# Kernel tuning notes

Hardware: AMD Instinct MI355X
Metric: run time of the kernel (lower is better)

Reference implementation:

```python
import jax, jax.numpy as jnp
import numpy as np

EPS = 1e-5
RATIO = (0.25, 0.25)
PATCH = (8, 8)
GROUPS = 8


def dct_matrix(N):
    # Orthonormal DCT-II matrix: dct_2d(x, norm='ortho') == C @ x @ C.T
    n = jnp.arange(N, dtype=jnp.float32)
    C = jnp.cos(jnp.pi * (n[None, :] + 0.5) * n[:, None] / N)
    s = jnp.where(n == 0, jnp.sqrt(1.0 / N), jnp.sqrt(2.0 / N))
    return C * s[:, None]


def dct2(x, Ch, Cw):
    y = jnp.einsum('uh,nchw->ncuw', Ch, x)
    return jnp.einsum('ncuw,vw->ncuv', y, Cw)


def idct2(x, Ch, Cw):
    y = jnp.einsum('hu,ncuv->nchv', Ch, x)
    return jnp.einsum('nchv,wv->nchw', y, Cw)


def conv2d(x, w, b=None, groups=1):
    y = jax.lax.conv_general_dilated(x, w, (1, 1), 'SAME',
        dimension_numbers=('NCHW', 'OIHW', 'NCHW'), feature_group_count=groups)
    return y if b is None else y + b[None, :, None, None]


def channel_norm(x, g, b):
    # GroupNorm with num_groups == num_channels (per-channel instance norm)
    mu = x.mean(axis=(2, 3), keepdims=True)
    var = ((x - mu) ** 2).mean(axis=(2, 3), keepdims=True)
    return (x - mu) * jax.lax.rsqrt(var + EPS) * g[None, :, None, None] + b[None, :, None, None]


def dwt(x):
    x01 = x[:, :, 0::2, :]
    x02 = x[:, :, 1::2, :]
    x1 = x01[:, :, :, 0::2]
    x2 = x02[:, :, :, 0::2]
    x3 = x01[:, :, :, 1::2]
    x4 = x02[:, :, :, 1::2]
    LL = (x1 + x2 + x3 + x4) / 4
    HL = (-x1 - x2 + x3 + x4) / 4
    LH = (-x1 + x2 - x3 + x4) / 4
    HH = (x1 - x2 - x3 + x4) / 4
    return LL, HL, LH, HH


def idwt(LL, HL, LH, HH):
    x1 = LL - HL - LH + HH
    x2 = LL - HL + LH - HH
    x3 = LL + HL - LH - HH
    x4 = LL + HL + LH + HH
    b, c, h, w = x1.shape
    upper = jnp.zeros((b, c, 2 * h, w), x1.dtype).at[:, :, 0::2, :].set(x1).at[:, :, 1::2, :].set(x2)
    lower = jnp.zeros((b, c, 2 * h, w), x1.dtype).at[:, :, 0::2, :].set(x3).at[:, :, 1::2, :].set(x4)
    return jnp.zeros((b, c, 2 * h, 2 * w), x1.dtype).at[:, :, :, 0::2].set(upper).at[:, :, :, 1::2].set(lower)


def freq_mask(h, w):
    h0, w0 = int(h * RATIO[0]), int(w * RATIO[1])
    return jnp.ones((h, w), jnp.float32).at[:h0, :w0].set(0.0)


def spatial_branch(x, noise_thr):
    LL, HL, LH, HH = dwt(x)
    h0, w0 = LL.shape[2], LL.shape[3]
    Ch, Cw = dct_matrix(h0), dct_matrix(w0)
    d = dct2(LL, Ch, Cw)
    d = jnp.where(jnp.abs(d) > noise_thr, jnp.tanh(d), d)
    d = d * freq_mask(h0, w0)[None, None]
    dct_ = idct2(d, Ch, Cw)
    return idwt(LL * dct_, HL * dct_, LH * dct_, HH * dct_)


def channel_branch(x, w_c1, w_c2):
    n, c, h, w = x.shape
    Ch, Cw = dct_matrix(h), dct_matrix(w)
    d = dct2(x, Ch, Cw) * freq_mask(h, w)[None, None]
    dct_ = idct2(d, Ch, Cw)
    ph, pw = PATCH
    blk = dct_.reshape(n, c, ph, h // ph, pw, w // pw)
    amaxp = blk.max(axis=(3, 5))   # adaptive max pool -> (n,c,8,8)
    aavgp = blk.mean(axis=(3, 5))  # adaptive avg pool -> (n,c,8,8)
    amaxp = jax.nn.gelu(amaxp, approximate=False).sum(axis=(2, 3))  # (n,c)
    aavgp = jax.nn.gelu(aavgp, approximate=False).sum(axis=(2, 3))
    # channel1x1 / channel2x1: depthwise 1x1 conv, no bias, mmcv ConvModule default ReLU
    channel = jax.nn.relu(w_c1[None, :] * amaxp) + jax.nn.relu(w_c1[None, :] * aavgp)
    gate = jax.nn.sigmoid(jax.nn.relu(w_c2[None, :] * channel))
    return x * gate[:, :, None, None]


def ema(x, w1, b1, w3, b3, gnw, gnb):
    b, c, h, w = x.shape
    cg = c // GROUPS
    gx = x.reshape(b * GROUPS, cg, h, w)
    x_h = gx.mean(axis=3, keepdims=True)                       # (bg,cg,h,1)
    x_w = gx.mean(axis=2, keepdims=True).transpose(0, 1, 3, 2)  # (bg,cg,w,1)
    hw = conv2d(jnp.concatenate([x_h, x_w], axis=2), w1, b1)   # 1x1 conv
    xh, xw = hw[:, :, :h, :], hw[:, :, h:, :]
    x1 = channel_norm(gx * jax.nn.sigmoid(xh) * jax.nn.sigmoid(xw.transpose(0, 1, 3, 2)), gnw, gnb)
    x2 = conv2d(gx, w3, b3)                                    # 3x3 conv
    x11 = jax.nn.softmax(x1.mean(axis=(2, 3)), axis=-1)[:, None, :]  # (bg,1,cg)
    x21 = jax.nn.softmax(x2.mean(axis=(2, 3)), axis=-1)[:, None, :]
    x12 = x2.reshape(b * GROUPS, cg, h * w)
    x22 = x1.reshape(b * GROUPS, cg, h * w)
    weights = (x11 @ x12 + x21 @ x22).reshape(b * GROUPS, 1, h, w)
    return (gx * jax.nn.sigmoid(weights)).reshape(b, c, h, w)


def setup_inputs() -> dict:
    key = jax.random.key(0)
    ks = jax.random.split(key, 6)
    B, C, H, W = 4, 64, 256, 256
    cg = C // GROUPS
    s = 0.05
    return {
        'x': jax.random.normal(ks[0], (B, C, H, W), jnp.float32),
        'noise_thr': jnp.asarray(0.1, jnp.float32),
        'w_c1': jax.random.normal(ks[1], (C,), jnp.float32) * s,
        'w_c2': jax.random.normal(ks[2], (C,), jnp.float32) * s,
        'w_out': jax.random.normal(ks[3], (C, C, 3, 3), jnp.float32) * s,
        'b_out': jnp.zeros((C,), jnp.float32),
        'gn_out_w': jnp.ones((C,), jnp.float32),
        'gn_out_b': jnp.zeros((C,), jnp.float32),
        'ema_w1': jax.random.normal(ks[4], (cg, cg, 1, 1), jnp.float32) * s,
        'ema_b1': jnp.zeros((cg,), jnp.float32),
        'ema_w3': jax.random.normal(ks[5], (cg, cg, 3, 3), jnp.float32) * s,
        'ema_b3': jnp.zeros((cg,), jnp.float32),
        'ema_gn_w': jnp.ones((cg,), jnp.float32),
        'ema_gn_b': jnp.zeros((cg,), jnp.float32),
    }


def reference(x, noise_thr, w_c1, w_c2, w_out, b_out, gn_out_w, gn_out_b,
              ema_w1, ema_b1, ema_w3, ema_b3, ema_gn_w, ema_gn_b):
    spatial = spatial_branch(x, noise_thr)
    channel = channel_branch(x, w_c1, w_c2)
    # HFP out: ConvModule(3x3, ReLU) -> GroupNorm(C, C)
    y = channel_norm(jax.nn.relu(conv2d(spatial + channel, w_out, b_out)), gn_out_w, gn_out_b)
    return ema(y, ema_w1, ema_b1, ema_w3, ema_b3, ema_gn_w, ema_gn_b)
```

## Files before the change

### kernel.cpp

```cpp
#include <hip/hip_runtime.h>
#include <math.h>

#define PI_F 3.14159274101257324f

#define OFF_C256   0u
#define OFF_C128   65536u
#define OFF_GATE   81920u
#define OFF_STATA  82176u
#define OFF_STATB  82432u
#define OFF_EMAA   82688u
#define OFF_EMAB   82944u
#define OFF_X2SUM  83200u
#define OFF_Q      83456u
#define OFF_R      83712u
#define OFF_P11    83744u
#define OFF_XH     83968u
#define OFF_XW     149504u
#define OFF_SH     215040u
#define OFF_SW     280576u
#define OFF_BIG    346112u


__global__ void k_dctmat(float* __restrict__ C256, float* __restrict__ C128) {
    int gid = blockIdx.x * 256 + threadIdx.x;
    if (gid < 65536) {
        int i = gid >> 8, j = gid & 255;
        float a = ((PI_F * ((float)j + 0.5f)) * (float)i) / 256.0f;
        float s = (i == 0) ? sqrtf(1.0f / 256.0f) : sqrtf(2.0f / 256.0f);
        C256[gid] = cosf(a) * s;
    } else if (gid < 65536 + 16384) {
        int g = gid - 65536;
        int i = g >> 7, j = g & 127;
        float a = ((PI_F * ((float)j + 0.5f)) * (float)i) / 128.0f;
        float s = (i == 0) ? sqrtf(1.0f / 128.0f) : sqrtf(2.0f / 128.0f);
        C128[g] = cosf(a) * s;
    }
}

__global__ void k_ll(const float* __restrict__ X, float* __restrict__ LL) {
    int gid = blockIdx.x * 256 + threadIdx.x;
    int img = gid >> 14, rem = gid & 16383;
    int i = rem >> 7, j = rem & 127;
    const float* base = X + (size_t)img * 65536;
    float2 a = *(const float2*)(base + (2 * i) * 256 + 2 * j);
    float2 b = *(const float2*)(base + (2 * i + 1) * 256 + 2 * j);
    LL[gid] = (a.x + a.y + b.x + b.y) * 0.25f;
}

template <int N, bool S1, int EPI>
__global__ __launch_bounds__(256) void k_gemm(const float* __restrict__ Cm,
                                              const float* __restrict__ In,
                                              float* __restrict__ Out,
                                              const float* __restrict__ thr_ptr) {
    __shared__ float As[16][68];
    __shared__ float Bs[16][68];
    const int tid = threadIdx.x;
    const int tx = tid & 15, ty = tid >> 4;
    const int j0 = blockIdx.x * 64, i0 = blockIdx.y * 64;
    const int b = blockIdx.z;
    const float* Inb = In + (size_t)b * N * N;

    float acc[4][4];
#pragma unroll
    for (int m = 0; m < 4; m++)
#pragma unroll
        for (int n = 0; n < 4; n++) acc[m][n] = 0.f;

    const int ra = tid >> 2;
    const int ka = (tid & 3) * 4;
    const int kb = tid >> 4;
    const int jb = (tid & 15) * 4;

    for (int k0 = 0; k0 < N; k0 += 16) {
        {
            const float* pa = S1 ? (Cm + (size_t)(i0 + ra) * N + k0 + ka)
                                 : (Inb + (size_t)(i0 + ra) * N + k0 + ka);
            float4 v = *(const float4*)pa;
            As[ka + 0][ra] = v.x; As[ka + 1][ra] = v.y;
            As[ka + 2][ra] = v.z; As[ka + 3][ra] = v.w;
        }
        if (S1) {
            const float* pb = Inb + (size_t)(k0 + kb) * N + j0 + jb;
            *(float4*)&Bs[kb][jb] = *(const float4*)pb;
        } else {
            const float* pb = Cm + (size_t)(j0 + ra) * N + k0 + ka;
            float4 v = *(const float4*)pb;
            Bs[ka + 0][ra] = v.x; Bs[ka + 1][ra] = v.y;
            Bs[ka + 2][ra] = v.z; Bs[ka + 3][ra] = v.w;
        }
        __syncthreads();
#pragma unroll
        for (int k = 0; k < 16; k++) {
            float4 a = *(const float4*)&As[k][ty * 4];
            float4 bb = *(const float4*)&Bs[k][tx * 4];
            float av[4] = {a.x, a.y, a.z, a.w};
            float bv[4] = {bb.x, bb.y, bb.z, bb.w};
#pragma unroll
            for (int m = 0; m < 4; m++)
#pragma unroll
                for (int n = 0; n < 4; n++) acc[m][n] = fmaf(av[m], bv[n], acc[m][n]);
        }
        __syncthreads();
    }

    float thr = 0.f;
    if (EPI == 1) thr = thr_ptr[0];
#pragma unroll
    for (int m = 0; m < 4; m++) {
        int gi = i0 + ty * 4 + m;
        float4 o;
        float* ov = (float*)&o;
#pragma unroll
        for (int n = 0; n < 4; n++) {
            int gj = j0 + tx * 4 + n;
            float v = acc[m][n];
            if (EPI == 1) {
                if (fabsf(v) > thr) v = tanhf(v);
                if (gi < N / 4 && gj < N / 4) v = 0.f;
            }
            ov[n] = v;
        }
        *(float4*)&Out[(size_t)b * N * N + (size_t)gi * N + j0 + tx * 4] = o;
    }
}

template <int M, int N, int K, int LDA, int LDB, bool TA, bool TB,
          long SA, long SB, int EPI>
__global__ __launch_bounds__(256) void k_bgemm(const float* __restrict__ A,
                                               const float* __restrict__ B,
                                               float* __restrict__ Out,
                                               const float* __restrict__ Xref) {
    __shared__ float As[16][68];
    __shared__ float Bs[16][68];
    const int tid = threadIdx.x;
    const int tx = tid & 15, ty = tid >> 4;
    const int j0 = blockIdx.x * 64, i0 = blockIdx.y * 64;
    const int b = blockIdx.z;
    const float* Ab = A + (size_t)b * (size_t)SA;
    const float* Bb = B + (size_t)b * (size_t)SB;

    float acc[4][4];
#pragma unroll
    for (int m = 0; m < 4; m++)
#pragma unroll
        for (int n = 0; n < 4; n++) acc[m][n] = 0.f;

    const int ra = tid >> 2;
    const int ka = (tid & 3) * 4;
    const int kb = tid >> 4;
    const int jb4 = (tid & 15) * 4;

    for (int k0 = 0; k0 < K; k0 += 16) {
        if (!TA) {
            float4 v = *(const float4*)(Ab + (size_t)(i0 + ra) * LDA + k0 + ka);
            As[ka + 0][ra] = v.x; As[ka + 1][ra] = v.y;
            As[ka + 2][ra] = v.z; As[ka + 3][ra] = v.w;
        } else {
            *(float4*)&As[kb][jb4] =
                *(const float4*)(Ab + (size_t)(k0 + kb) * LDA + i0 + jb4);
        }
        if (!TB) {
            *(float4*)&Bs[kb][jb4] =
                *(const float4*)(Bb + (size_t)(k0 + kb) * LDB + j0 + jb4);
        } else {
            float4 v = *(const float4*)(Bb + (size_t)(j0 + ra) * LDB + k0 + ka);
            Bs[ka + 0][ra] = v.x; Bs[ka + 1][ra] = v.y;
            Bs[ka + 2][ra] = v.z; Bs[ka + 3][ra] = v.w;
        }
        __syncthreads();
#pragma unroll
        for (int k = 0; k < 16; k++) {
            float4 a = *(const float4*)&As[k][ty * 4];
            float4 bb = *(const float4*)&Bs[k][tx * 4];
            float av[4] = {a.x, a.y, a.z, a.w};
            float bv[4] = {bb.x, bb.y, bb.z, bb.w};
#pragma unroll
            for (int m = 0; m < 4; m++)
#pragma unroll
                for (int n = 0; n < 4; n++) acc[m][n] = fmaf(av[m], bv[n], acc[m][n]);
        }
        __syncthreads();
    }

#pragma unroll
    for (int m = 0; m < 4; m++) {
        size_t rowoff = (size_t)b * (size_t)M * N + (size_t)(i0 + ty * 4 + m) * N + j0 + tx * 4;
        float4 o;
        if (EPI == 3) {
            float4 xr = *(const float4*)&Xref[rowoff];
            o.x = xr.x - acc[m][0]; o.y = xr.y - acc[m][1];
            o.z = xr.z - acc[m][2]; o.w = xr.w - acc[m][3];
        } else {
            o.x = acc[m][0]; o.y = acc[m][1]; o.z = acc[m][2]; o.w = acc[m][3];
        }
        *(float4*)&Out[rowoff] = o;
    }
}

__global__ __launch_bounds__(256) void k_pool_gate(const float* __restrict__ D,
                                                   const float* __restrict__ wc1,
                                                   const float* __restrict__ wc2,
                                                   float* __restrict__ gate) {
    __shared__ float redM[4], redA[4];
    const int img = blockIdx.x;
    const int c = img & 63;
    const int tid = threadIdx.x, lane = tid & 63, wid = tid >> 6;
    const int t = tid >> 2;
    const int sub = tid & 3;
    const int tr = t >> 3, tc = t & 7;
    const float* base = D + (size_t)img * 65536 + (size_t)(tr * 32 + sub * 8) * 256 + tc * 32;

    float mx = -3.4e38f, sum = 0.f;
#pragma unroll
    for (int r = 0; r < 8; r++) {
#pragma unroll
        for (int c4 = 0; c4 < 8; c4++) {
            float4 v = *(const float4*)(base + (size_t)r * 256 + 4 * c4);
            mx = fmaxf(mx, fmaxf(fmaxf(v.x, v.y), fmaxf(v.z, v.w)));
            sum += v.x + v.y + v.z + v.w;
        }
    }
    mx = fmaxf(mx, __shfl_xor(mx, 1)); sum += __shfl_xor(sum, 1);
    mx = fmaxf(mx, __shfl_xor(mx, 2)); sum += __shfl_xor(sum, 2);

    float gM = 0.f, gA = 0.f;
    if (sub == 0) {
        float mean = sum * (1.f / 1024.f);
        gM = 0.5f * mx * (1.f + erff(mx * 0.70710678118654752f));
        gA = 0.5f * mean * (1.f + erff(mean * 0.70710678118654752f));
    }
    for (int o = 32; o; o >>= 1) { gM += __shfl_down(gM, o); gA += __shfl_down(gA, o); }
    if (lane == 0) { redM[wid] = gM; redA[wid] = gA; }
    __syncthreads();
    if (tid == 0) {
        float accM = redM[0] + redM[1] + redM[2] + redM[3];
        float accA = redA[0] + redA[1] + redA[2] + redA[3];
        float c1 = wc1[c], c2 = wc2[c];
        float ch = fmaxf(c1 * accM, 0.f) + fmaxf(c1 * accA, 0.f);
        float g = fmaxf(c2 * ch, 0.f);
        gate[img] = 1.f / (1.f + expf(-g));
    }
}

__global__ void k_zassm(const float* __restrict__ X, const float* __restrict__ D2,
                        const float* __restrict__ gate, float* __restrict__ Z) {
    int gid = blockIdx.x * 256 + threadIdx.x;
    int img = gid >> 14, rem = gid & 16383;
    int h = rem >> 6, w4 = (rem & 63) * 4;
    float4 xv = *((const float4*)(X + (size_t)img * 65536 + (size_t)h * 256) + (rem & 63));
    float2 dd = *(const float2*)(D2 + (size_t)img * 16384 + (h >> 1) * 128 + (w4 >> 1));
    float g = gate[img];
    float4 o;
    o.x = xv.x * (dd.x + g); o.y = xv.y * (dd.x + g);
    o.z = xv.z * (dd.y + g); o.w = xv.w * (dd.y + g);
    *((float4*)(Z + (size_t)img * 65536 + (size_t)h * 256) + (rem & 63)) = o;
}

template <int CIN, bool RELU, bool DOSUM>
__global__ __launch_bounds__(256, 4) void k_conv3(const float* __restrict__ In,
                                                  const float* __restrict__ W,
                                                  const float* __restrict__ Bias,
                                                  float* __restrict__ Out,
                                                  float* __restrict__ SumOut) {
    __shared__ float sIn[8][34][37];
    __shared__ float rb[4];
    const int bz = blockIdx.z;
    int nImg, co0;
    if (CIN == 64) { nImg = bz >> 3; co0 = (bz & 7) * 8; }
    else           { nImg = bz;      co0 = 0; }
    const size_t inbase  = (size_t)nImg * CIN * 65536;
    const size_t outbase = (size_t)nImg * ((CIN == 64) ? 64 : 8) * 65536;
    const int y0 = blockIdx.y * 32, x0 = blockIdx.x * 32;
    const int tid = threadIdx.x;
    const int row = tid >> 3;
    const int tx  = tid & 7;
    const int cL  = (tx == 0) ? 33 : 4 * tx - 1;

    float acc[8][4];
#pragma unroll
    for (int a = 0; a < 8; a++)
#pragma unroll
        for (int n = 0; n < 4; n++) acc[a][n] = 0.f;

    for (int cc = 0; cc < CIN / 8; ++cc) {
        if (cc) __syncthreads();
        for (int t = tid; t < 272; t += 256) {
            int ci = t / 34, iy = t % 34;
            int gy = y0 + iy - 1;
            float* dst = &sIn[ci][iy][0];
            if (gy >= 0 && gy < 256) {
                const float* src = In + inbase + (size_t)(cc * 8 + ci) * 65536 + (size_t)gy * 256;
#pragma unroll
                for (int jb = 0; jb < 8; jb++) {
                    float4 v = *(const float4*)(src + x0 + 4 * jb);
                    dst[4 * jb + 0] = v.x; dst[4 * jb + 1] = v.y;
                    dst[4 * jb + 2] = v.z; dst[4 * jb + 3] = v.w;
                }
                dst[32] = (x0 + 32 < 256) ? src[x0 + 32] : 0.f;
                dst[33] = (x0 - 1 >= 0)  ? src[x0 - 1]  : 0.f;
            } else {
#pragma unroll
                for (int j = 0; j < 34; j++) dst[j] = 0.f;
            }
        }
        __syncthreads();

        const float* Wc = W + ((size_t)co0 * CIN + (size_t)cc * 8) * 9;
        for (int ci = 0; ci < 8; ++ci) {
            for (int ky = 0; ky < 3; ++ky) {
                const int iy = row + ky;
                const float* rowp = &sIn[ci][iy][0];
                float win[6];
                win[0] = rowp[cL];
                win[1] = rowp[4 * tx + 0];
                win[2] = rowp[4 * tx + 1];
                win[3] = rowp[4 * tx + 2];
                win[4] = rowp[4 * tx + 3];
                win[5] = rowp[4 * tx + 4];
#pragma unroll
                for (int co = 0; co < 8; ++co) {
                    const float* wp = Wc + ((size_t)co * CIN + ci) * 9 + ky * 3;
                    float wa = wp[0], wb = wp[1], wc = wp[2];
#pragma unroll
                    for (int n = 0; n < 4; ++n)
                        acc[co][n] = fmaf(wa, win[n],
                                     fmaf(wb, win[n + 1],
                                     fmaf(wc, win[n + 2], acc[co][n])));
                }
            }
        }
    }

#pragma unroll
    for (int co = 0; co < 8; ++co) {
        float bsv = Bias[co0 + co];
        float4 o;
        o.x = acc[co][0] + bsv; o.y = acc[co][1] + bsv;
        o.z = acc[co][2] + bsv; o.w = acc[co][3] + bsv;
        if (RELU) {
            o.x = fmaxf(o.x, 0.f); o.y = fmaxf(o.y, 0.f);
            o.z = fmaxf(o.z, 0.f); o.w = fmaxf(o.w, 0.f);
        }
        *(float4*)&Out[outbase + (size_t)(co0 + co) * 65536 +
                       (size_t)(y0 + row) * 256 + x0 + 4 * tx] = o;
    }

    if (DOSUM) {
        const int lane = tid & 63, wid = tid >> 6;
        for (int co = 0; co < 8; co++) {
            float s = acc[co][0] + acc[co][1] + acc[co][2] + acc[co][3] +
                      4.f * Bias[co0 + co];
            for (int o = 32; o; o >>= 1) s += __shfl_down(s, o);
            if (lane == 0) rb[wid] = s;
            __syncthreads();
            if (tid == 0) atomicAdd(&SumOut[nImg * 8 + co], rb[0] + rb[1] + rb[2] + rb[3]);
            __syncthreads();
        }
    }
}

__global__ __launch_bounds__(256) void k_cnstats(const float* __restrict__ X,
                                                 const float* __restrict__ gw,
                                                 const float* __restrict__ gb,
                                                 float* __restrict__ A, float* __restrict__ B) {
    __shared__ float s1b[4], s2b[4];
    const int img = blockIdx.x;
    const float* base = X + (size_t)img * 65536;
    const int tid = threadIdx.x, lane = tid & 63, wid = tid >> 6;
    float s = 0.f, s2 = 0.f;
    for (int i = tid; i < 16384; i += 256) {
        float4 v = ((const float4*)base)[i];
        s += v.x + v.y + v.z + v.w;
        s2 += v.x * v.x + v.y * v.y + v.z * v.z + v.w * v.w;
    }
    for (int o = 32; o; o >>= 1) { s += __shfl_down(s, o); s2 += __shfl_down(s2, o); }
    if (lane == 0) { s1b[wid] = s; s2b[wid] = s2; }
    __syncthreads();
    if (tid == 0) {
        float S = s1b[0] + s1b[1] + s1b[2] + s1b[3];
        float S2 = s2b[0] + s2b[1] + s2b[2] + s2b[3];
        float mu = S * (1.f / 65536.f);
        float var = S2 * (1.f / 65536.f) - mu * mu;
        float al = gw[img & 63] * rsqrtf(var + 1e-5f);
        A[img] = al;
        B[img] = gb[img & 63] - mu * al;
    }
}

__global__ void k_cnapply(const float* __restrict__ X, const float* __restrict__ A,
                          const float* __restrict__ B, float* __restrict__ Y) {
    int gid = blockIdx.x * 256 + threadIdx.x;
    int img = gid >> 14;
    float a = A[img], b = B[img];
    float4 v = ((const float4*)X)[gid];
    float4 o = {fmaf(a, v.x, b), fmaf(a, v.y, b), fmaf(a, v.z, b), fmaf(a, v.w, b)};
    ((float4*)Y)[gid] = o;
}

__global__ void k_rowmean(const float* __restrict__ Y, float* __restrict__ XH) {
    int row = blockIdx.x * 4 + (threadIdx.x >> 6);
    int lane = threadIdx.x & 63;
    float4 v = ((const float4*)(Y + (size_t)row * 256))[lane];
    float s = v.x + v.y + v.z + v.w;
    for (int o = 32; o; o >>= 1) s += __shfl_down(s, o);
    if (lane == 0) XH[row] = s * (1.f / 256.f);
}

__global__ void k_colmean(const float* __restrict__ Y, float* __restrict__ XW) {
    int gid = blockIdx.x * 256 + threadIdx.x;
    int img = gid >> 8, w = gid & 255;
    const float* p = Y + (size_t)img * 65536 + w;
    float s = 0.f;
    for (int h = 0; h < 256; h++) s += p[h * 256];
    XW[gid] = s * (1.f / 256.f);
}

__global__ void k_hw1x1(const float* __restrict__ XH, const float* __restrict__ XW,
                        const float* __restrict__ W1, const float* __restrict__ B1,
                        float* __restrict__ SH, float* __restrict__ SW) {
    int gid = blockIdx.x * 256 + threadIdx.x;
    int half = gid >> 16;
    int rem = gid & 65535;
    int bg = rem >> 11, r2 = rem & 2047, co = r2 >> 8, p = r2 & 255;
    const float* src = (half ? XW : XH) + bg * 2048 + p;
    float s = B1[co];
#pragma unroll
    for (int ci = 0; ci < 8; ci++) s = fmaf(W1[co * 8 + ci], src[ci * 256], s);
    float sig = 1.f / (1.f + expf(-s));
    (half ? SW : SH)[bg * 2048 + co * 256 + p] = sig;
}

__global__ __launch_bounds__(256) void k_emastats(const float* __restrict__ Y,
                                                  const float* __restrict__ SH,
                                                  const float* __restrict__ SW,
                                                  const float* __restrict__ gnw,
                                                  const float* __restrict__ gnb,
                                                  float* __restrict__ A, float* __restrict__ B) {
    __shared__ float s1b[4], s2b[4];
    const int img = blockIdx.x;
    const int bg = img >> 3, ci = img & 7;
    const float* base = Y + (size_t)img * 65536;
    const float* sh = SH + bg * 2048 + ci * 256;
    const float* sw = SW + bg * 2048 + ci * 256;
    const int tid = threadIdx.x, lane = tid & 63, wid = tid >> 6;
    float s = 0.f, s2 = 0.f;
    for (int i = tid; i < 65536; i += 256) {
        int h = i >> 8, w = i & 255;
        float t = base[i] * sh[h] * sw[w];
        s += t;
        s2 += t * t;
    }
    for (int o = 32; o; o >>= 1) { s += __shfl_down(s, o); s2 += __shfl_down(s2, o); }
    if (lane == 0) { s1b[wid] = s; s2b[wid] = s2; }
    __syncthreads();
    if (tid == 0) {
        float S = s1b[0] + s1b[1] + s1b[2] + s1b[3];
        float S2 = s2b[0] + s2b[1] + s2b[2] + s2b[3];
        float mu = S * (1.f / 65536.f);
        float var = S2 * (1.f / 65536.f) - mu * mu;
        float al = gnw[ci] * rsqrtf(var + 1e-5f);
        A[img] = al;
        B[img] = gnb[ci] - mu * al;
    }
}

__global__ void k_ema_smalls(const float* __restrict__ X2S, const float* __restrict__ EA,
                             const float* __restrict__ EB, const float* __restrict__ gnb,
                             float* __restrict__ Q, float* __restrict__ R,
                             float* __restrict__ P11) {
    int tid = threadIdx.x;
    int ci = tid & 7;
    float m2 = X2S[tid] * (1.f / 65536.f);
    float mx = m2;
    mx = fmaxf(mx, __shfl_xor(mx, 1, 8));
    mx = fmaxf(mx, __shfl_xor(mx, 2, 8));
    mx = fmaxf(mx, __shfl_xor(mx, 4, 8));
    float e = expf(m2 - mx);
    float se = e;
    se += __shfl_xor(se, 1, 8); se += __shfl_xor(se, 2, 8); se += __shfl_xor(se, 4, 8);
    float x21 = e / se;
    Q[tid] = x21 * EA[tid];
    float rt = x21 * EB[tid];
    rt += __shfl_xor(rt, 1, 8); rt += __shfl_xor(rt, 2, 8); rt += __shfl_xor(rt, 4, 8);
    if (ci == 0) R[tid >> 3] = rt;
    float g = gnb[ci];
    float gm = g;
    gm = fmaxf(gm, __shfl_xor(gm, 1, 8));
    gm = fmaxf(gm, __shfl_xor(gm, 2, 8));
    gm = fmaxf(gm, __shfl_xor(gm, 4, 8));
    float ge = expf(g - gm);
    float gs = ge;
    gs += __shfl_xor(gs, 1, 8); gs += __shfl_xor(gs, 2, 8); gs += __shfl_xor(gs, 4, 8);
    if (tid < 8) P11[tid] = ge / gs;
}

__global__ __launch_bounds__(256) void k_ema_final(const float* __restrict__ Y,
                                                   const float* X2,
                                                   const float* __restrict__ SH,
                                                   const float* __restrict__ SW,
                                                   const float* __restrict__ P11,
                                                   const float* __restrict__ Q,
                                                   const float* __restrict__ R,
                                                   float* Out) {
    int gid = blockIdx.x * 256 + threadIdx.x;
    int bg = gid >> 14, rem = gid & 16383;
    int h = rem >> 6, w4i = rem & 63;
    float4 ys[8];
    float rv = R[bg];
    float4 acc = {rv, rv, rv, rv};
#pragma unroll
    for (int ci = 0; ci < 8; ci++) {
        size_t base = ((size_t)(bg * 8 + ci)) * 65536 + (size_t)h * 256;
        float4 yv = ((const float4*)(Y + base))[w4i];
        float4 xv = ((const float4*)(X2 + base))[w4i];
        ys[ci] = yv;
        float p = P11[ci], q = Q[bg * 8 + ci];
        float shv = SH[bg * 2048 + ci * 256 + h];
        float4 swv = ((const float4*)(SW + bg * 2048 + ci * 256))[w4i];
        float qs = q * shv;
        acc.x += p * xv.x + qs * yv.x * swv.x;
        acc.y += p * xv.y + qs * yv.y * swv.y;
        acc.z += p * xv.z + qs * yv.z * swv.z;
        acc.w += p * xv.w + qs * yv.w * swv.w;
    }
    float4 sg;
    sg.x = 1.f / (1.f + expf(-acc.x));
    sg.y = 1.f / (1.f + expf(-acc.y));
    sg.z = 1.f / (1.f + expf(-acc.z));
    sg.w = 1.f / (1.f + expf(-acc.w));
#pragma unroll
    for (int ci = 0; ci < 8; ci++) {
        float4 o = {ys[ci].x * sg.x, ys[ci].y * sg.y, ys[ci].z * sg.z, ys[ci].w * sg.w};
        ((float4*)(Out + ((size_t)(bg * 8 + ci)) * 65536 + (size_t)h * 256))[w4i] = o;
    }
}

extern "C" void kernel_launch(void* const* d_in, const int* in_sizes, int n_in,
                              void* d_out, int out_size, void* d_ws, size_t ws_size,
                              hipStream_t stream) {
    (void)in_sizes; (void)n_in; (void)out_size; (void)ws_size;
    const float* x     = (const float*)d_in[0];
    const float* thr   = (const float*)d_in[1];
    const float* w_c1  = (const float*)d_in[2];
    const float* w_c2  = (const float*)d_in[3];
    const float* w_out = (const float*)d_in[4];
    const float* b_out = (const float*)d_in[5];
    const float* gn_w  = (const float*)d_in[6];
    const float* gn_b  = (const float*)d_in[7];
    const float* ew1   = (const float*)d_in[8];
    const float* eb1   = (const float*)d_in[9];
    const float* ew3   = (const float*)d_in[10];
    const float* eb3   = (const float*)d_in[11];
    const float* egw   = (const float*)d_in[12];
    const float* egb   = (const float*)d_in[13];

    float* ws   = (float*)d_ws;
    float* C256 = ws + OFF_C256;
    float* C128 = ws + OFF_C128;
    float* GATE = ws + OFF_GATE;
    float* SA_A = ws + OFF_STATA;
    float* SA_B = ws + OFF_STATB;
    float* EMAA = ws + OFF_EMAA;
    float* EMAB = ws + OFF_EMAB;
    float* X2S  = ws + OFF_X2SUM;
    float* Qb   = ws + OFF_Q;
    float* Rb   = ws + OFF_R;
    float* P11b = ws + OFF_P11;
    float* XH   = ws + OFF_XH;
    float* XW   = ws + OFF_XW;
    float* SHp  = ws + OFF_SH;
    float* SWp  = ws + OFF_SW;
    float* BIG  = ws + OFF_BIG;

    float* DO  = (float*)d_out;
    float* Ubuf = DO;
    float* Vbuf = DO + 4194304;
    float* Wbuf = DO + 5242880;
    float* LLb = DO;
    float* T1  = DO + 4194304;
    float* T2  = DO + 8388608;

    k_dctmat<<<320, 256, 0, stream>>>(C256, C128);

    k_bgemm<64, 256, 256, 256, 256, false, false, 0, 65536, 0>
        <<<dim3(4, 1, 256), 256, 0, stream>>>(C256, x, Ubuf, nullptr);
    k_bgemm<64, 64, 256, 256, 256, false, true, 16384, 0, 0>
        <<<dim3(1, 1, 256), 256, 0, stream>>>(Ubuf, C256, Vbuf, nullptr);
    k_bgemm<256, 64, 64, 256, 64, true, false, 0, 4096, 0>
        <<<dim3(1, 4, 256), 256, 0, stream>>>(C256, Vbuf, Wbuf, nullptr);
    k_bgemm<256, 256, 64, 64, 256, false, false, 16384, 0, 3>
        <<<dim3(4, 4, 256), 256, 0, stream>>>(Wbuf, C256, BIG, x);
    k_pool_gate<<<256, 256, 0, stream>>>(BIG, w_c1, w_c2, GATE);

    k_ll<<<16384, 256, 0, stream>>>(x, LLb);
    k_gemm<128, true, 0><<<dim3(2, 2, 256), 256, 0, stream>>>(C128, LLb, T1, nullptr);
    k_gemm<128, false, 1><<<dim3(2, 2, 256), 256, 0, stream>>>(C128, T1, T2, thr);
    k_gemm<128, true, 0><<<dim3(2, 2, 256), 256, 0, stream>>>(C128, T2, T1, nullptr);
    k_gemm<128, false, 0><<<dim3(2, 2, 256), 256, 0, stream>>>(C128, T1, T2, nullptr);

    k_zassm<<<16384, 256, 0, stream>>>(x, T2, GATE, BIG);

    k_conv3<64, true, false><<<dim3(8, 8, 32), 256, 0, stream>>>(BIG, w_out, b_out, DO, nullptr);
    k_cnstats<<<256, 256, 0, stream>>>(DO, gn_w, gn_b, SA_A, SA_B);
    k_cnapply<<<16384, 256, 0, stream>>>(DO, SA_A, SA_B, BIG);

    k_rowmean<<<16384, 256, 0, stream>>>(BIG, XH);
    k_colmean<<<256, 256, 0, stream>>>(BIG, XW);
    k_hw1x1<<<512, 256, 0, stream>>>(XH, XW, ew1, eb1, SHp, SWp);
    k_emastats<<<256, 256, 0, stream>>>(BIG, SHp, SWp, egw, egb, EMAA, EMAB);
    hipMemsetAsync(X2S, 0, 256 * sizeof(float), stream);
    k_conv3<8, false, true><<<dim3(8, 8, 32), 256, 0, stream>>>(BIG, ew3, eb3, DO, X2S);
    k_ema_smalls<<<1, 256, 0, stream>>>(X2S, EMAA, EMAB, egb, Qb, Rb, P11b);
    k_ema_final<<<2048, 256, 0, stream>>>(BIG, DO, SHp, SWp, P11b, Qb, Rb, (float*)d_out);
}
```

Measured before the change: 830.7 us.

## Prefetch next input-channel chunk into registers while computing 3x3 conv

The 3x3 conv kernel now stages 4 input channels per step instead of 8 and uses register double-buffering. Global loads for the next chunk are issued before the current chunk's FMA loop and written to shared memory afterward. This aims to hide global-memory latency behind compute and shrink the shared-memory footprint. In exchange it doubles the number of barrier-separated steps and adds about 34 prefetch registers per staging thread, which may cause spills or reduce occupancy.

New measurement: 1.363 ms. 64.1% more time.

```diff
diff --git a/kernel.cpp b/kernel.cpp
--- a/kernel.cpp
+++ b/kernel.cpp
@@ -262,7 +262,7 @@
                                                   const float* __restrict__ Bias,
                                                   float* __restrict__ Out,
                                                   float* __restrict__ SumOut) {
-    __shared__ float sIn[8][34][37];
+    __shared__ float sIn[4][34][37];
     __shared__ float rb[4];
     const int bz = blockIdx.z;
     int nImg, co0;
@@ -276,37 +276,57 @@
     const int tx  = tid & 7;
     const int cL  = (tx == 0) ? 33 : 4 * tx - 1;
 
-    float acc[8][4];
-#pragma unroll
-    for (int a = 0; a < 8; a++)
-#pragma unroll
-        for (int n = 0; n < 4; n++) acc[a][n] = 0.f;
-
-    for (int cc = 0; cc < CIN / 8; ++cc) {
-        if (cc) __syncthreads();
-        for (int t = tid; t < 272; t += 256) {
-            int ci = t / 34, iy = t % 34;
-            int gy = y0 + iy - 1;
-            float* dst = &sIn[ci][iy][0];
-            if (gy >= 0 && gy < 256) {
-                const float* src = In + inbase + (size_t)(cc * 8 + ci) * 65536 + (size_t)gy * 256;
+    const bool stager = tid < 136;
+    const int sci = stager ? tid / 34 : 0;
+    const int siy = stager ? tid % 34 : 0;
+    const int sgy = y0 + siy - 1;
+    const bool rowok = stager && sgy >= 0 && sgy < 256;
+
+    constexpr int NCC = CIN / 4;
+
+    float4 pf[8];
+    float pfA = 0.f, pfB = 0.f;
+
+    auto LOAD = [&](int cc) {
+        if (rowok) {
+            const float* src = In + inbase + (size_t)(cc * 4 + sci) * 65536 + (size_t)sgy * 256;
+#pragma unroll
+            for (int jb = 0; jb < 8; jb++) pf[jb] = *(const float4*)(src + x0 + 4 * jb);
+            pfA = (x0 + 32 < 256) ? src[x0 + 32] : 0.f;
+            pfB = (x0 - 1 >= 0)  ? src[x0 - 1]  : 0.f;
+        }
+    };
+    auto STORE = [&]() {
+        if (stager) {
+            float* dst = &sIn[sci][siy][0];
+            if (rowok) {
 #pragma unroll
                 for (int jb = 0; jb < 8; jb++) {
-                    float4 v = *(const float4*)(src + x0 + 4 * jb);
-                    dst[4 * jb + 0] = v.x; dst[4 * jb + 1] = v.y;
-                    dst[4 * jb + 2] = v.z; dst[4 * jb + 3] = v.w;
+                    dst[4 * jb + 0] = pf[jb].x; dst[4 * jb + 1] = pf[jb].y;
+                    dst[4 * jb + 2] = pf[jb].z; dst[4 * jb + 3] = pf[jb].w;
                 }
-                dst[32] = (x0 + 32 < 256) ? src[x0 + 32] : 0.f;
-                dst[33] = (x0 - 1 >= 0)  ? src[x0 - 1]  : 0.f;
+                dst[32] = pfA; dst[33] = pfB;
             } else {
 #pragma unroll
                 for (int j = 0; j < 34; j++) dst[j] = 0.f;
             }
         }
+    };
+
+    float acc[8][4];
+#pragma unroll
+    for (int a = 0; a < 8; a++)
+#pragma unroll
+        for (int n = 0; n < 4; n++) acc[a][n] = 0.f;
+
+    LOAD(0);
+    STORE();
+    for (int cc = 0; cc < NCC; ++cc) {
         __syncthreads();
-
-        const float* Wc = W + ((size_t)co0 * CIN + (size_t)cc * 8) * 9;
-        for (int ci = 0; ci < 8; ++ci) {
+        if (cc + 1 < NCC) LOAD(cc + 1);
+
+        const float* Wc = W + ((size_t)co0 * CIN + (size_t)cc * 4) * 9;
+        for (int ci = 0; ci < 4; ++ci) {
             for (int ky = 0; ky < 3; ++ky) {
                 const int iy = row + ky;
                 const float* rowp = &sIn[ci][iy][0];
@@ -328,6 +348,11 @@
                                      fmaf(wc, win[n + 2], acc[co][n])));
                 }
             }
+        }
+
+        if (cc + 1 < NCC) {
+            __syncthreads();
+            STORE();
         }
     }
 
```
